# Performance work log

Hardware: AMD Instinct MI355X
Metric: run time of the kernel (lower is better)

## Reference

```python
import jax, jax.numpy as jnp
import numpy as np

N = 100000
E = 1600000
IN_C, HID_C, OUT_C = 128, 256, 40


def sage_conv(x, src, dst, W_l, W_r, b):
    # mean aggregation of source-node features into destination nodes
    msgs = x[src]                                            # [E, d]
    agg = jax.ops.segment_sum(msgs, dst, num_segments=N)     # [N, d]
    deg = jax.ops.segment_sum(jnp.ones((src.shape[0],), x.dtype), dst,
                              num_segments=N)                # [N]
    agg = agg / jnp.clip(deg, 1.0, None)[:, None]
    # out = lin_l(agg) + lin_r(x); weights stored [out, in] like torch
    return agg @ W_l.T + x @ W_r.T + b


def setup_inputs() -> dict:
    key = jax.random.key(0)
    ks = jax.random.split(key, 10)
    s = 0.05
    x = jax.random.normal(ks[0], (N, IN_C), dtype=jnp.float32)
    edge_index = jax.random.randint(ks[1], (2, E), 0, N, dtype=jnp.int64)
    return {
        "x": x,
        "edge_index": edge_index,
        "W_l0": jax.random.normal(ks[2], (HID_C, IN_C), dtype=jnp.float32) * s,
        "W_r0": jax.random.normal(ks[3], (HID_C, IN_C), dtype=jnp.float32) * s,
        "b0": jnp.zeros((HID_C,), jnp.float32),
        "W_l1": jax.random.normal(ks[4], (HID_C, HID_C), dtype=jnp.float32) * s,
        "W_r1": jax.random.normal(ks[5], (HID_C, HID_C), dtype=jnp.float32) * s,
        "b1": jnp.zeros((HID_C,), jnp.float32),
        "W_lo": jax.random.normal(ks[6], (OUT_C, HID_C), dtype=jnp.float32) * s,
        "W_ro": jax.random.normal(ks[7], (OUT_C, HID_C), dtype=jnp.float32) * s,
        "bo": jnp.zeros((OUT_C,), jnp.float32),
    }


def reference(x, edge_index, W_l0, W_r0, b0, W_l1, W_r1, b1, W_lo, W_ro, bo):
    src, dst = edge_index[0], edge_index[1]
    h = jax.nn.relu(sage_conv(x, src, dst, W_l0, W_r0, b0))
    h = jax.nn.relu(sage_conv(h, src, dst, W_l1, W_r1, b1))
    out = sage_conv(h, src, dst, W_lo, W_ro, bo)
    return jax.nn.log_softmax(out, axis=1)
```

## Files before the change

kernel.cpp:

```cpp
#include <hip/hip_runtime.h>
#include <hip/hip_bf16.h>
#include <cstdint>
#include <cstddef>

#define NN   100000
#define NE   1600000
#define HID  256
#define OUTC 40

typedef __attribute__((ext_vector_type(8))) short bf16x8;
typedef __attribute__((ext_vector_type(4))) float f32x4;

static __device__ __forceinline__ ushort f2bf(float f) {
    __hip_bfloat16 h = __float2bfloat16(f);
    return *reinterpret_cast<ushort*>(&h);
}
static __device__ __forceinline__ float bflo(unsigned u) { return __uint_as_float(u << 16); }
static __device__ __forceinline__ float bfhi(unsigned u) { return __uint_as_float(u & 0xffff0000u); }
static __device__ __forceinline__ float ubf(unsigned w, int k) {
    return (float)((w >> (8 * k)) & 255u);
}

__global__ void k_count(const int* __restrict__ dst, int* __restrict__ cnt) {
    int i = blockIdx.x * blockDim.x + threadIdx.x;
    if (i < NE) atomicAdd(&cnt[dst[i]], 1);
}

__global__ void k_blocksum(const int* __restrict__ cnt, int* __restrict__ bsum) {
    __shared__ int s[256];
    int t = threadIdx.x;
    int n = blockIdx.x * 256 + t;
    s[t] = (n < NN) ? cnt[n] : 0;
    __syncthreads();
    for (int off = 128; off; off >>= 1) {
        if (t < off) s[t] += s[t + off];
        __syncthreads();
    }
    if (t == 0) bsum[blockIdx.x] = s[0];
}

__global__ void k_scanblock(const int* __restrict__ bsum, int* __restrict__ boff, int nb) {
    __shared__ int s[512];
    int t = threadIdx.x;
    int v = (t < nb) ? bsum[t] : 0;
    s[t] = v;
    __syncthreads();
    for (int off = 1; off < 512; off <<= 1) {
        int u = (t >= off) ? s[t - off] : 0;
        __syncthreads();
        s[t] += u;
        __syncthreads();
    }
    if (t < nb) boff[t] = s[t] - v;
}

__global__ void k_rowptr(const int* __restrict__ cnt, const int* __restrict__ boff,
                         int* __restrict__ rowptr, int* __restrict__ fillp,
                         float* __restrict__ invd) {
    __shared__ int s[256];
    int t = threadIdx.x;
    int n = blockIdx.x * 256 + t;
    int c = (n < NN) ? cnt[n] : 0;
    s[t] = c;
    __syncthreads();
    for (int off = 1; off < 256; off <<= 1) {
        int u = (t >= off) ? s[t - off] : 0;
        __syncthreads();
        s[t] += u;
        __syncthreads();
    }
    if (n < NN) {
        int excl = boff[blockIdx.x] + s[t] - c;
        rowptr[n] = excl;
        fillp[n]  = excl;
        invd[n]   = 1.0f / (float)(c > 1 ? c : 1);
    }
    if (n == 0) rowptr[NN] = NE;
}

__global__ void k_fill(const int* __restrict__ src, const int* __restrict__ dst,
                       int* __restrict__ fillp, int* __restrict__ colidx) {
    int i = blockIdx.x * blockDim.x + threadIdx.x;
    if (i < NE) {
        int p = atomicAdd(&fillp[dst[i]], 1);
        colidx[p] = src[i];
    }
}

__global__ void k_cvtfrag(const float* __restrict__ W, ushort* __restrict__ dst,
                          int ocreal, int d, int nf) {
    int f = blockIdx.x * 256 + threadIdx.x;
    if (f >= nf) return;
    int lm = f & 15, lk = (f >> 4) & 3;
    int rest = f >> 6;
    int dk = d / 32;
    int kk = rest % dk, cc = rest / dk;
    int row = cc * 16 + lm, col = kk * 32 + lk * 8;
    unsigned q0 = 0, q1 = 0, q2 = 0, q3 = 0;
    if (row < ocreal) {
        const float4* p = (const float4*)(W + (size_t)row * d + col);
        float4 a = p[0], b = p[1];
        q0 = (unsigned)f2bf(a.x) | ((unsigned)f2bf(a.y) << 16);
        q1 = (unsigned)f2bf(a.z) | ((unsigned)f2bf(a.w) << 16);
        q2 = (unsigned)f2bf(b.x) | ((unsigned)f2bf(b.y) << 16);
        q3 = (unsigned)f2bf(b.z) | ((unsigned)f2bf(b.w) << 16);
    }
    *(uint4*)(dst + (size_t)f * 8) = make_uint4(q0, q1, q2, q3);
}

__global__ __launch_bounds__(256) void k_quant_x8(const float* __restrict__ x,
                                                  unsigned char* __restrict__ xq,
                                                  float* __restrict__ sx) {
    int t = threadIdx.x;
    int qw = t >> 4, ql = t & 15;
    int row = blockIdx.x * 16 + qw;
    if (row >= NN) return;
    const float4* p = (const float4*)(x + (size_t)row * 128 + ql * 8);
    float4 a = p[0], b = p[1];
    float v[8] = {a.x, a.y, a.z, a.w, b.x, b.y, b.z, b.w};
    float m = 0.f;
    #pragma unroll
    for (int k = 0; k < 8; ++k) m = fmaxf(m, fabsf(v[k]));
    m = fmaxf(m, __shfl_xor(m, 1));
    m = fmaxf(m, __shfl_xor(m, 2));
    m = fmaxf(m, __shfl_xor(m, 4));
    m = fmaxf(m, __shfl_xor(m, 8));
    float inv = (m > 0.f) ? 127.f / m : 0.f;
    unsigned w0 = 0, w1 = 0;
    #pragma unroll
    for (int k = 0; k < 4; ++k)
        w0 |= ((unsigned)((int)rintf(v[k] * inv) + 128) & 255u) << (8 * k);
    #pragma unroll
    for (int k = 0; k < 4; ++k)
        w1 |= ((unsigned)((int)rintf(v[4 + k] * inv) + 128) & 255u) << (8 * k);
    *(uint2*)(xq + (size_t)row * 128 + ql * 8) = make_uint2(w0, w1);
    if (ql == 0) sx[row] = (m > 0.f) ? m / 127.f : 0.f;
}

__global__ __launch_bounds__(256) void k_quant_h8(const ushort* __restrict__ h,
                                                  unsigned char* __restrict__ hq,
                                                  float* __restrict__ s8) {
    int t = threadIdx.x;
    int qw = t >> 4, ql = t & 15;
    int row = blockIdx.x * 16 + qw;
    if (row >= NN) return;
    const uint4* p = (const uint4*)(h + (size_t)row * 256 + ql * 16);
    uint4 a = p[0], b = p[1];
    float v[16];
    v[0]  = bflo(a.x); v[1]  = bfhi(a.x); v[2]  = bflo(a.y); v[3]  = bfhi(a.y);
    v[4]  = bflo(a.z); v[5]  = bfhi(a.z); v[6]  = bflo(a.w); v[7]  = bfhi(a.w);
    v[8]  = bflo(b.x); v[9]  = bfhi(b.x); v[10] = bflo(b.y); v[11] = bfhi(b.y);
    v[12] = bflo(b.z); v[13] = bfhi(b.z); v[14] = bflo(b.w); v[15] = bfhi(b.w);
    float m = 0.f;
    #pragma unroll
    for (int k = 0; k < 16; ++k) m = fmaxf(m, v[k]);
    m = fmaxf(m, __shfl_xor(m, 1));
    m = fmaxf(m, __shfl_xor(m, 2));
    m = fmaxf(m, __shfl_xor(m, 4));
    m = fmaxf(m, __shfl_xor(m, 8));
    float inv = (m > 0.f) ? 255.f / m : 0.f;
    unsigned wo[4];
    #pragma unroll
    for (int wi = 0; wi < 4; ++wi) {
        unsigned w = 0;
        #pragma unroll
        for (int k = 0; k < 4; ++k)
            w |= ((unsigned)(int)rintf(v[wi * 4 + k] * inv) & 255u) << (8 * k);
        wo[wi] = w;
    }
    *(uint4*)(hq + (size_t)row * 256 + ql * 16) = make_uint4(wo[0], wo[1], wo[2], wo[3]);
    if (ql == 0) s8[row] = (m > 0.f) ? m / 255.f : 0.f;
}

template<int D, bool SELF_F32, bool BIASED>
__global__ __launch_bounds__(256, 4) void k_layer8u(
    const unsigned char* __restrict__ qin, const float* __restrict__ qs,
    const float* __restrict__ xf,
    const ushort* __restrict__ Wl, const ushort* __restrict__ Wr,
    const float* __restrict__ bias, const float* __restrict__ invd,
    const int* __restrict__ rowptr, const int* __restrict__ colidx,
    ushort* __restrict__ hout)
{
    __shared__ ushort aggS[64 * D];
    __shared__ int cidxS[2048];
    char* aggSb = (char*)aggS;
    const int t  = threadIdx.x;
    const int r0 = blockIdx.x * 64;
    constexpr int LPR = D / 16;
    constexpr int GPB = 256 / LPR;
    constexpr int RSH = (D == 128) ? 7 : 8;
    const int gid = t / LPR, li = t % LPR;
    const int l = t & 63;
    const int base = l & ~(LPR - 1);

    const int ebase = rowptr[r0];
    const int rend  = (r0 + 64 < NN) ? (r0 + 64) : NN;
    const int etot  = rowptr[rend] - ebase;
    const bool inlds = (etot <= 2048);
    if (inlds) {
        for (int i = t; i < etot; i += 256) cidxS[i] = colidx[ebase + i];
    }
    __syncthreads();

    for (int rr = gid; rr < 64; rr += GPB) {
        const int r = r0 + rr;
        float acc[16];
        #pragma unroll
        for (int k = 0; k < 16; ++k) acc[k] = 0.f;
        float sum_sc = 0.f;
        if (r < NN) {
            const int beg = rowptr[r], end = rowptr[r + 1];
            for (int e = beg; e < end; e += 8) {
                const int myi = e + (li & 7);
                int se = -1;
                if (myi < end) se = inlds ? cidxS[myi - ebase] : colidx[myi];
                float mysc = (se >= 0) ? qs[se] : 0.f;
                int   sj[8];
                float sc[8];
                uint4 u[8];
                #pragma unroll
                for (int j = 0; j < 8; ++j) sj[j] = __shfl(se, base + j);
                #pragma unroll
                for (int j = 0; j < 8; ++j) sc[j] = __shfl(mysc, base + j);
                #pragma unroll
                for (int j = 0; j < 8; ++j) {
                    u[j] = (sj[j] >= 0)
                        ? *(const uint4*)(qin + (((unsigned)sj[j]) << RSH) + (li << 4))
                        : make_uint4(0u, 0u, 0u, 0u);
                }
                #pragma unroll
                for (int j = 0; j < 8; ++j) {
                    #pragma unroll
                    for (int wi = 0; wi < 4; ++wi) {
                        unsigned w = (&u[j].x)[wi];
                        acc[wi*4+0] = fmaf(sc[j], ubf(w, 0), acc[wi*4+0]);
                        acc[wi*4+1] = fmaf(sc[j], ubf(w, 1), acc[wi*4+1]);
                        acc[wi*4+2] = fmaf(sc[j], ubf(w, 2), acc[wi*4+2]);
                        acc[wi*4+3] = fmaf(sc[j], ubf(w, 3), acc[wi*4+3]);
                    }
                    if (BIASED) sum_sc += sc[j];
                }
            }
            const float iv = invd[r];
            #pragma unroll
            for (int k = 0; k < 16; ++k) {
                if (BIASED) acc[k] = (acc[k] - 128.f * sum_sc) * iv;
                else        acc[k] = acc[k] * iv;
            }
        }
        #pragma unroll
        for (int gg = 0; gg < 2; ++gg) {
            unsigned q0 = (unsigned)f2bf(acc[gg*8+0]) | ((unsigned)f2bf(acc[gg*8+1]) << 16);
            unsigned q1 = (unsigned)f2bf(acc[gg*8+2]) | ((unsigned)f2bf(acc[gg*8+3]) << 16);
            unsigned q2 = (unsigned)f2bf(acc[gg*8+4]) | ((unsigned)f2bf(acc[gg*8+5]) << 16);
            unsigned q3 = (unsigned)f2bf(acc[gg*8+6]) | ((unsigned)f2bf(acc[gg*8+7]) << 16);
            int g  = li * 2 + gg;
            int gs = g ^ (rr & 7);
            *(uint4*)(aggSb + (size_t)rr * (D * 2) + (gs << 4)) = make_uint4(q0, q1, q2, q3);
        }
    }
    __syncthreads();

    const int w = t >> 6, lm = l & 15, lk = l >> 4;
    const int rr = w * 16 + lm;
    const int rg = r0 + rr;

    bf16x8 ax[D / 32];
    if (SELF_F32) {
        #pragma unroll
        for (int kk = 0; kk < D / 32; ++kk) {
            bf16x8 v;
            if (rg < NN) {
                const float4* p = (const float4*)(xf + (size_t)rg * D + kk * 32 + lk * 8);
                float4 f0 = p[0], f1 = p[1];
                v[0] = (short)f2bf(f0.x); v[1] = (short)f2bf(f0.y);
                v[2] = (short)f2bf(f0.z); v[3] = (short)f2bf(f0.w);
                v[4] = (short)f2bf(f1.x); v[5] = (short)f2bf(f1.y);
                v[6] = (short)f2bf(f1.z); v[7] = (short)f2bf(f1.w);
            } else v = (bf16x8)(short)0;
            ax[kk] = v;
        }
    } else {
        const float sr = (rg < NN) ? qs[rg] : 0.f;
        #pragma unroll
        for (int kk = 0; kk < D / 32; ++kk) {
            uint2 uq = (rg < NN)
                ? *(const uint2*)(qin + (((unsigned)rg) << RSH) + kk * 32 + lk * 8)
                : make_uint2(0u, 0u);
            bf16x8 v;
            v[0] = (short)f2bf(sr * ubf(uq.x, 0));
            v[1] = (short)f2bf(sr * ubf(uq.x, 1));
            v[2] = (short)f2bf(sr * ubf(uq.x, 2));
            v[3] = (short)f2bf(sr * ubf(uq.x, 3));
            v[4] = (short)f2bf(sr * ubf(uq.y, 0));
            v[5] = (short)f2bf(sr * ubf(uq.y, 1));
            v[6] = (short)f2bf(sr * ubf(uq.y, 2));
            v[7] = (short)f2bf(sr * ubf(uq.y, 3));
            ax[kk] = v;
        }
    }

    for (int cc = 0; cc < HID / 16; ++cc) {
        const int c = cc * 16 + lm;
        f32x4 acc = {0.f, 0.f, 0.f, 0.f};
        #pragma unroll
        for (int kk = 0; kk < D / 32; ++kk) {
            int g  = kk * 4 + lk;
            int gs = g ^ (rr & 7);
            bf16x8 a_agg = *(const bf16x8*)(aggSb + (size_t)rr * (D * 2) + (gs << 4));
            const size_t wf = ((size_t)(cc * (D / 32) + kk) * 64 + l) * 8;
            bf16x8 bl = *(const bf16x8*)(Wl + wf);
            bf16x8 br = *(const bf16x8*)(Wr + wf);
            acc = __builtin_amdgcn_mfma_f32_16x16x32_bf16(a_agg, bl, acc, 0, 0, 0);
            acc = __builtin_amdgcn_mfma_f32_16x16x32_bf16(ax[kk], br, acc, 0, 0, 0);
        }
        const float bv = bias[c];
        #pragma unroll
        for (int i = 0; i < 4; ++i) {
            const int orow = r0 + w * 16 + lk * 4 + i;
            if (orow < NN) {
                float v = fmaxf(acc[i] + bv, 0.f);
                hout[(size_t)orow * HID + c] = f2bf(v);
            }
        }
    }
}

__global__ __launch_bounds__(256, 4) void k_premul(
    const ushort* __restrict__ h1, const ushort* __restrict__ wlo,
    const ushort* __restrict__ wro, const float* __restrict__ bo,
    unsigned char* __restrict__ qq, float* __restrict__ sq, float* __restrict__ rbuf)
{
    const int t = threadIdx.x;
    const int r0 = blockIdx.x * 64;
    const int w = t >> 6, l = t & 63, lm = l & 15, lk = l >> 4;
    const int rr = w * 16 + lm;
    const int rg = r0 + rr;

    f32x4 aq[3], ar[3];
    #pragma unroll
    for (int cc = 0; cc < 3; ++cc) { aq[cc] = {0.f,0.f,0.f,0.f}; ar[cc] = {0.f,0.f,0.f,0.f}; }

    #pragma unroll
    for (int kk = 0; kk < 8; ++kk) {
        bf16x8 a = (rg < NN)
            ? *(const bf16x8*)(h1 + (size_t)rg * 256 + kk * 32 + lk * 8)
            : (bf16x8)(short)0;
        #pragma unroll
        for (int cc = 0; cc < 3; ++cc) {
            const size_t wf = ((size_t)(cc * 8 + kk) * 64 + l) * 8;
            bf16x8 bl = *(const bf16x8*)(wlo + wf);
            bf16x8 br = *(const bf16x8*)(wro + wf);
            aq[cc] = __builtin_amdgcn_mfma_f32_16x16x32_bf16(a, bl, aq[cc], 0, 0, 0);
            ar[cc] = __builtin_amdgcn_mfma_f32_16x16x32_bf16(a, br, ar[cc], 0, 0, 0);
        }
    }

    #pragma unroll
    for (int i = 0; i < 4; ++i) {
        const int orow = r0 + w * 16 + lk * 4 + i;
        if (orow >= NN) continue;
        float m = 0.f;
        #pragma unroll
        for (int cc = 0; cc < 3; ++cc) {
            const int c = cc * 16 + lm;
            if (c < OUTC) m = fmaxf(m, fabsf(aq[cc][i]));
        }
        m = fmaxf(m, __shfl_xor(m, 1));
        m = fmaxf(m, __shfl_xor(m, 2));
        m = fmaxf(m, __shfl_xor(m, 4));
        m = fmaxf(m, __shfl_xor(m, 8));
        const float inv = (m > 0.f) ? 127.f / m : 0.f;
        #pragma unroll
        for (int cc = 0; cc < 3; ++cc) {
            const int c = cc * 16 + lm;
            int code = (c < OUTC) ? (int)rintf(aq[cc][i] * inv) : 0;
            qq[(size_t)orow * 64 + c] = (unsigned char)(code + 128);
            rbuf[(size_t)orow * 64 + c] = (c < OUTC) ? (ar[cc][i] + bo[c]) : 0.f;
        }
        qq[(size_t)orow * 64 + 48 + lm] = (unsigned char)128;
        rbuf[(size_t)orow * 64 + 48 + lm] = 0.f;
        if (lm == 0) sq[orow] = m / 127.f;
    }
}

__global__ __launch_bounds__(256) void k_final(
    const unsigned char* __restrict__ qq, const float* __restrict__ sq,
    const float* __restrict__ rbuf, const float* __restrict__ invd,
    const int* __restrict__ rowptr, const int* __restrict__ colidx,
    float* __restrict__ out)
{
    __shared__ int cidxS[2048];
    const int t = threadIdx.x;
    const int g = t >> 2, li = t & 3;
    const int r0 = blockIdx.x * 64;
    const int row = r0 + g;
    const int l = t & 63;
    const int base = l & ~3;

    const int ebase = rowptr[r0];
    const int rend  = (r0 + 64 < NN) ? (r0 + 64) : NN;
    const int etot  = rowptr[rend] - ebase;
    const bool inlds = (etot <= 2048);
    if (inlds) {
        for (int i = t; i < etot; i += 256) cidxS[i] = colidx[ebase + i];
    }
    __syncthreads();
    if (row >= NN) return;

    float acc[16];
    #pragma unroll
    for (int k = 0; k < 16; ++k) acc[k] = 0.f;
    float sum_sc = 0.f;

    const int beg = rowptr[row], end = rowptr[row + 1];
    for (int e = beg; e < end; e += 8) {
        const int m0 = e + li, m1 = e + 4 + li;
        int se0 = -1, se1 = -1;
        if (m0 < end) se0 = inlds ? cidxS[m0 - ebase] : colidx[m0];
        if (m1 < end) se1 = inlds ? cidxS[m1 - ebase] : colidx[m1];
        float ms0 = (se0 >= 0) ? sq[se0] : 0.f;
        float ms1 = (se1 >= 0) ? sq[se1] : 0.f;
        int   sj[8];
        float sc[8];
        uint4 u[8];
        #pragma unroll
        for (int j = 0; j < 4; ++j) { sj[j] = __shfl(se0, base + j); sc[j] = __shfl(ms0, base + j); }
        #pragma unroll
        for (int j = 4; j < 8; ++j) { sj[j] = __shfl(se1, base + j - 4); sc[j] = __shfl(ms1, base + j - 4); }
        #pragma unroll
        for (int j = 0; j < 8; ++j) {
            u[j] = (sj[j] >= 0)
                ? *(const uint4*)(qq + (((unsigned)sj[j]) << 6) + (li << 4))
                : make_uint4(0u, 0u, 0u, 0u);
        }
        #pragma unroll
        for (int j = 0; j < 8; ++j) {
            #pragma unroll
            for (int wi = 0; wi < 4; ++wi) {
                unsigned w = (&u[j].x)[wi];
                acc[wi*4+0] = fmaf(sc[j], ubf(w, 0), acc[wi*4+0]);
                acc[wi*4+1] = fmaf(sc[j], ubf(w, 1), acc[wi*4+1]);
                acc[wi*4+2] = fmaf(sc[j], ubf(w, 2), acc[wi*4+2]);
                acc[wi*4+3] = fmaf(sc[j], ubf(w, 3), acc[wi*4+3]);
            }
            sum_sc += sc[j];
        }
    }

    const float iv = invd[row];
    const float4* rp = (const float4*)(rbuf + (size_t)row * 64 + li * 16);
    float v[16];
    #pragma unroll
    for (int ch = 0; ch < 4; ++ch) {
        float4 rv = rp[ch];
        v[ch*4+0] = (acc[ch*4+0] - 128.f * sum_sc) * iv + rv.x;
        v[ch*4+1] = (acc[ch*4+1] - 128.f * sum_sc) * iv + rv.y;
        v[ch*4+2] = (acc[ch*4+2] - 128.f * sum_sc) * iv + rv.z;
        v[ch*4+3] = (acc[ch*4+3] - 128.f * sum_sc) * iv + rv.w;
    }
    #pragma unroll
    for (int k = 0; k < 16; ++k)
        if (li * 16 + k >= OUTC) v[k] = -INFINITY;

    float m = v[0];
    #pragma unroll
    for (int k = 1; k < 16; ++k) m = fmaxf(m, v[k]);
    m = fmaxf(m, __shfl_xor(m, 1));
    m = fmaxf(m, __shfl_xor(m, 2));

    float s = 0.f;
    #pragma unroll
    for (int k = 0; k < 16; ++k)
        if (li * 16 + k < OUTC) s += __expf(v[k] - m);
    s += __shfl_xor(s, 1);
    s += __shfl_xor(s, 2);
    const float ls = __logf(s);

    #pragma unroll
    for (int ch = 0; ch < 4; ++ch) {
        const int c = li * 16 + ch * 4;
        if (c < OUTC) {
            float4 o;
            o.x = v[ch*4+0] - m - ls;
            o.y = v[ch*4+1] - m - ls;
            o.z = v[ch*4+2] - m - ls;
            o.w = v[ch*4+3] - m - ls;
            *(float4*)(out + (size_t)row * OUTC + c) = o;
        }
    }
}

extern "C" void kernel_launch(void* const* d_in, const int* in_sizes, int n_in,
                              void* d_out, int out_size, void* d_ws, size_t ws_size,
                              hipStream_t stream) {
    const float* x   = (const float*)d_in[0];
    const int*   ei  = (const int*)d_in[1];
    const int*   src = ei;
    const int*   dst = ei + NE;
    const float* Wl0 = (const float*)d_in[2];
    const float* Wr0 = (const float*)d_in[3];
    const float* b0  = (const float*)d_in[4];
    const float* Wl1 = (const float*)d_in[5];
    const float* Wr1 = (const float*)d_in[6];
    const float* b1  = (const float*)d_in[7];
    const float* Wlo = (const float*)d_in[8];
    const float* Wro = (const float*)d_in[9];
    const float* bo  = (const float*)d_in[10];
    float* out = (float*)d_out;

    char* ws = (char*)d_ws;
    const size_t MB = 1 << 20;
    float*         invd   = (float*)(ws + 0);
    int*           rowptr = (int*)(ws + MB / 2);
    int*           cnt    = (int*)(ws + MB);
    int*           fillp  = (int*)(ws + MB + MB / 2);
    int*           bsum   = (int*)(ws + 2 * MB);
    int*           boff   = (int*)(ws + 2 * MB + MB / 4);
    float*         sx     = (float*)(ws + 2 * MB + MB / 2);
    float*         s8     = (float*)(ws + 3 * MB);
    float*         sq     = (float*)(ws + 4 * MB);
    ushort*        Wb     = (ushort*)(ws + 4 * MB + MB / 2);
    int*           colidx = (int*)(ws + 5 * MB + MB / 2);
    unsigned char* xq8    = (unsigned char*)(ws + 12 * MB);
    unsigned char* qq     = (unsigned char*)(ws + 12 * MB);
    ushort*        h0     = (ushort*)(ws + 32 * MB);
    ushort*        h1     = (ushort*)(ws + 32 * MB);
    unsigned char* h0q8u  = (unsigned char*)(ws + 84 * MB);
    float*         rbuf   = (float*)(ws + 84 * MB);

    ushort* wl0 = Wb;
    ushort* wr0 = Wb + 32768;
    ushort* wl1 = Wb + 65536;
    ushort* wr1 = Wb + 131072;
    ushort* wlo = Wb + 196608;
    ushort* wro = Wb + 208896;

    hipMemsetAsync(cnt, 0, NN * sizeof(int), stream);
    k_count<<<(NE + 255) / 256, 256, 0, stream>>>(dst, cnt);
    const int NB = (NN + 255) / 256;
    k_blocksum<<<NB, 256, 0, stream>>>(cnt, bsum);
    k_scanblock<<<1, 512, 0, stream>>>(bsum, boff, NB);
    k_rowptr<<<NB, 256, 0, stream>>>(cnt, boff, rowptr, fillp, invd);
    k_fill<<<(NE + 255) / 256, 256, 0, stream>>>(src, dst, fillp, colidx);

    k_cvtfrag<<<16, 256, 0, stream>>>(Wl0, wl0, 256, 128, 4096);
    k_cvtfrag<<<16, 256, 0, stream>>>(Wr0, wr0, 256, 128, 4096);
    k_cvtfrag<<<32, 256, 0, stream>>>(Wl1, wl1, 256, 256, 8192);
    k_cvtfrag<<<32, 256, 0, stream>>>(Wr1, wr1, 256, 256, 8192);
    k_cvtfrag<<<6,  256, 0, stream>>>(Wlo, wlo, 40, 256, 1536);
    k_cvtfrag<<<6,  256, 0, stream>>>(Wro, wro, 40, 256, 1536);
    k_quant_x8<<<(NN + 15) / 16, 256, 0, stream>>>(x, xq8, sx);

    const int GB = (NN + 63) / 64;
    k_layer8u<128, true, true><<<GB, 256, 0, stream>>>(
        xq8, sx, x, wl0, wr0, b0, invd, rowptr, colidx, h0);
    k_quant_h8<<<(NN + 15) / 16, 256, 0, stream>>>(h0, h0q8u, s8);
    k_layer8u<256, false, false><<<GB, 256, 0, stream>>>(
        h0q8u, s8, nullptr, wl1, wr1, b1, invd, rowptr, colidx, h1);
    k_premul<<<GB, 256, 0, stream>>>(h1, wlo, wro, bo, qq, sq, rbuf);
    k_final<<<(NN + 63) / 64, 256, 0, stream>>>(qq, sq, rbuf, invd, rowptr, colidx, out);
}
```

Before: 513.4 us.

## Shrink layer-kernel row tiles and split output columns across waves

The layer kernels now process fewer rows per block (32 rows for D=128, 16 for D=256) so that each thread group aggregates exactly one row, and shared memory shrinks accordingly. In the MFMA stage the waves split the output columns instead of each owning a 16-row tile, and the launch bounds are raised to allow more resident blocks. The aim is more blocks and higher occupancy for the latency-bound gather. In exchange, weight fragments are reloaded by more blocks, there are more launches' worth of blocks, and the column-index cache in shared memory is smaller.

```diff
diff --git a/kernel.cpp b/kernel.cpp
--- a/kernel.cpp
+++ b/kernel.cpp
@@ -173,7 +173,7 @@
 }
 
 template<int D, bool SELF_F32, bool BIASED>
-__global__ __launch_bounds__(256, 4) void k_layer8u(
+__global__ __launch_bounds__(256, 6) void k_layer8u(
     const unsigned char* __restrict__ qin, const float* __restrict__ qs,
     const float* __restrict__ xf,
     const ushort* __restrict__ Wl, const ushort* __restrict__ Wr,
@@ -181,28 +181,33 @@
     const int* __restrict__ rowptr, const int* __restrict__ colidx,
     ushort* __restrict__ hout)
 {
-    __shared__ ushort aggS[64 * D];
-    __shared__ int cidxS[2048];
+    constexpr int R   = 4096 / D;
+    constexpr int LPR = D / 16;
+    constexpr int RSH = (D == 128) ? 7 : 8;
+    constexpr int NRT = R / 16;
+    constexpr int WPRT = 4 / NRT;
+    constexpr int CCW  = 16 / WPRT;
+
+    __shared__ ushort aggS[R * D];
+    __shared__ int cidxS[1024];
     char* aggSb = (char*)aggS;
     const int t  = threadIdx.x;
-    const int r0 = blockIdx.x * 64;
-    constexpr int LPR = D / 16;
-    constexpr int GPB = 256 / LPR;
-    constexpr int RSH = (D == 128) ? 7 : 8;
+    const int r0 = blockIdx.x * R;
     const int gid = t / LPR, li = t % LPR;
     const int l = t & 63;
     const int base = l & ~(LPR - 1);
 
     const int ebase = rowptr[r0];
-    const int rend  = (r0 + 64 < NN) ? (r0 + 64) : NN;
+    const int rend  = (r0 + R < NN) ? (r0 + R) : NN;
     const int etot  = rowptr[rend] - ebase;
-    const bool inlds = (etot <= 2048);
+    const bool inlds = (etot <= 1024);
     if (inlds) {
         for (int i = t; i < etot; i += 256) cidxS[i] = colidx[ebase + i];
     }
     __syncthreads();
 
-    for (int rr = gid; rr < 64; rr += GPB) {
+    {
+        const int rr = gid;
         const int r = r0 + rr;
         float acc[16];
         #pragma unroll
@@ -262,7 +267,9 @@
     __syncthreads();
 
     const int w = t >> 6, lm = l & 15, lk = l >> 4;
-    const int rr = w * 16 + lm;
+    const int rt  = w / WPRT;
+    const int cc0 = (w % WPRT) * CCW;
+    const int rr = rt * 16 + lm;
     const int rg = r0 + rr;
 
     bf16x8 ax[D / 32];
@@ -300,7 +307,9 @@
         }
     }
 
-    for (int cc = 0; cc < HID / 16; ++cc) {
+    #pragma unroll
+    for (int ccl = 0; ccl < CCW; ++ccl) {
+        const int cc = cc0 + ccl;
         const int c = cc * 16 + lm;
         f32x4 acc = {0.f, 0.f, 0.f, 0.f};
         #pragma unroll
@@ -317,7 +326,7 @@
         const float bv = bias[c];
         #pragma unroll
         for (int i = 0; i < 4; ++i) {
-            const int orow = r0 + w * 16 + lk * 4 + i;
+            const int orow = r0 + rt * 16 + lk * 4 + i;
             if (orow < NN) {
                 float v = fmaxf(acc[i] + bv, 0.f);
                 hout[(size_t)orow * HID + c] = f2bf(v);
@@ -552,12 +561,11 @@
     k_cvtfrag<<<6,  256, 0, stream>>>(Wro, wro, 40, 256, 1536);
     k_quant_x8<<<(NN + 15) / 16, 256, 0, stream>>>(x, xq8, sx);
 
-    const int GB = (NN + 63) / 64;
-    k_layer8u<128, true, true><<<GB, 256, 0, stream>>>(
+    k_layer8u<128, true, true><<<(NN + 31) / 32, 256, 0, stream>>>(
         xq8, sx, x, wl0, wr0, b0, invd, rowptr, colidx, h0);
     k_quant_h8<<<(NN + 15) / 16, 256, 0, stream>>>(h0, h0q8u, s8);
-    k_layer8u<256, false, false><<<GB, 256, 0, stream>>>(
+    k_layer8u<256, false, false><<<(NN + 15) / 16, 256, 0, stream>>>(
         h0q8u, s8, nullptr, wl1, wr1, b1, invd, rowptr, colidx, h1);
-    k_premul<<<GB, 256, 0, stream>>>(h1, wlo, wro, bo, qq, sq, rbuf);
+    k_premul<<<(NN + 63) / 64, 256, 0, stream>>>(h1, wlo, wro, bo, qq, sq, rbuf);
     k_final<<<(NN + 63) / 64, 256, 0, stream>>>(qq, sq, rbuf, invd, rowptr, colidx, out);
 }
```

Result: slower. 536.2 us (+4.4%).

## Fuse h0 quantization into layer0 and output premul into layer1 epilogue

Applied to the files above, without the earlier changes.

The layer-0 kernel now quantizes its ReLU output to uint8 per row directly in the MFMA epilogue, so the separate bf16 h0 write and the quantize pass are gone. The layer-1 kernel writes its ReLU output into shared memory and performs the output-layer premultiply in place, so the bf16 h1 round-trip and the premul launch are gone. The MFMA loops are restructured to hold all 16 output-column accumulators at once and reuse each A fragment across columns, with occupancy lowered to 3 blocks per SM. The risks are higher register pressure and byte-wise scattered global stores of the quantized output.

```diff
diff --git a/kernel.cpp b/kernel.cpp
--- a/kernel.cpp
+++ b/kernel.cpp
@@ -137,61 +137,20 @@
     if (ql == 0) sx[row] = (m > 0.f) ? m / 127.f : 0.f;
 }
 
-__global__ __launch_bounds__(256) void k_quant_h8(const ushort* __restrict__ h,
-                                                  unsigned char* __restrict__ hq,
-                                                  float* __restrict__ s8) {
-    int t = threadIdx.x;
-    int qw = t >> 4, ql = t & 15;
-    int row = blockIdx.x * 16 + qw;
-    if (row >= NN) return;
-    const uint4* p = (const uint4*)(h + (size_t)row * 256 + ql * 16);
-    uint4 a = p[0], b = p[1];
-    float v[16];
-    v[0]  = bflo(a.x); v[1]  = bfhi(a.x); v[2]  = bflo(a.y); v[3]  = bfhi(a.y);
-    v[4]  = bflo(a.z); v[5]  = bfhi(a.z); v[6]  = bflo(a.w); v[7]  = bfhi(a.w);
-    v[8]  = bflo(b.x); v[9]  = bfhi(b.x); v[10] = bflo(b.y); v[11] = bfhi(b.y);
-    v[12] = bflo(b.z); v[13] = bfhi(b.z); v[14] = bflo(b.w); v[15] = bfhi(b.w);
-    float m = 0.f;
-    #pragma unroll
-    for (int k = 0; k < 16; ++k) m = fmaxf(m, v[k]);
-    m = fmaxf(m, __shfl_xor(m, 1));
-    m = fmaxf(m, __shfl_xor(m, 2));
-    m = fmaxf(m, __shfl_xor(m, 4));
-    m = fmaxf(m, __shfl_xor(m, 8));
-    float inv = (m > 0.f) ? 255.f / m : 0.f;
-    unsigned wo[4];
-    #pragma unroll
-    for (int wi = 0; wi < 4; ++wi) {
-        unsigned w = 0;
-        #pragma unroll
-        for (int k = 0; k < 4; ++k)
-            w |= ((unsigned)(int)rintf(v[wi * 4 + k] * inv) & 255u) << (8 * k);
-        wo[wi] = w;
-    }
-    *(uint4*)(hq + (size_t)row * 256 + ql * 16) = make_uint4(wo[0], wo[1], wo[2], wo[3]);
-    if (ql == 0) s8[row] = (m > 0.f) ? m / 255.f : 0.f;
-}
-
-template<int D, bool SELF_F32, bool BIASED>
-__global__ __launch_bounds__(256, 4) void k_layer8u(
-    const unsigned char* __restrict__ qin, const float* __restrict__ qs,
+__global__ __launch_bounds__(256, 3) void k_layer0(
+    const unsigned char* __restrict__ xq, const float* __restrict__ sx,
     const float* __restrict__ xf,
     const ushort* __restrict__ Wl, const ushort* __restrict__ Wr,
     const float* __restrict__ bias, const float* __restrict__ invd,
     const int* __restrict__ rowptr, const int* __restrict__ colidx,
-    ushort* __restrict__ hout)
+    unsigned char* __restrict__ hq, float* __restrict__ hs)
 {
-    __shared__ ushort aggS[64 * D];
+    __shared__ ushort aggS[64 * 128];
     __shared__ int cidxS[2048];
     char* aggSb = (char*)aggS;
     const int t  = threadIdx.x;
     const int r0 = blockIdx.x * 64;
-    constexpr int LPR = D / 16;
-    constexpr int GPB = 256 / LPR;
-    constexpr int RSH = (D == 128) ? 7 : 8;
-    const int gid = t / LPR, li = t % LPR;
     const int l = t & 63;
-    const int base = l & ~(LPR - 1);
 
     const int ebase = rowptr[r0];
     const int rend  = (r0 + 64 < NN) ? (r0 + 64) : NN;
@@ -202,61 +161,62 @@
     }
     __syncthreads();
 
-    for (int rr = gid; rr < 64; rr += GPB) {
-        const int r = r0 + rr;
-        float acc[16];
-        #pragma unroll
-        for (int k = 0; k < 16; ++k) acc[k] = 0.f;
-        float sum_sc = 0.f;
-        if (r < NN) {
-            const int beg = rowptr[r], end = rowptr[r + 1];
-            for (int e = beg; e < end; e += 8) {
-                const int myi = e + (li & 7);
-                int se = -1;
-                if (myi < end) se = inlds ? cidxS[myi - ebase] : colidx[myi];
-                float mysc = (se >= 0) ? qs[se] : 0.f;
-                int   sj[8];
-                float sc[8];
-                uint4 u[8];
+    {
+        const int gid = t >> 3, li = t & 7;
+        const int base = l & ~7;
+        for (int rr = gid; rr < 64; rr += 32) {
+            const int r = r0 + rr;
+            float acc[16];
+            #pragma unroll
+            for (int k = 0; k < 16; ++k) acc[k] = 0.f;
+            float sum_sc = 0.f;
+            if (r < NN) {
+                const int beg = rowptr[r], end = rowptr[r + 1];
+                for (int e = beg; e < end; e += 8) {
+                    const int myi = e + li;
+                    int se = -1;
+                    if (myi < end) se = inlds ? cidxS[myi - ebase] : colidx[myi];
+                    float mysc = (se >= 0) ? sx[se] : 0.f;
+                    int   sj[8];
+                    float sc[8];
+                    uint4 u[8];
+                    #pragma unroll
+                    for (int j = 0; j < 8; ++j) sj[j] = __shfl(se, base + j);
+                    #pragma unroll
+                    for (int j = 0; j < 8; ++j) sc[j] = __shfl(mysc, base + j);
+                    #pragma unroll
+                    for (int j = 0; j < 8; ++j) {
+                        u[j] = (sj[j] >= 0)
+                            ? *(const uint4*)(xq + (((unsigned)sj[j]) << 7) + (li << 4))
+                            : make_uint4(0u, 0u, 0u, 0u);
+                    }
+                    #pragma unroll
+                    for (int j = 0; j < 8; ++j) {
+                        #pragma unroll
+                        for (int wi = 0; wi < 4; ++wi) {
+                            unsigned w = (&u[j].x)[wi];
+                            acc[wi*4+0] = fmaf(sc[j], ubf(w, 0), acc[wi*4+0]);
+                            acc[wi*4+1] = fmaf(sc[j], ubf(w, 1), acc[wi*4+1]);
+                            acc[wi*4+2] = fmaf(sc[j], ubf(w, 2), acc[wi*4+2]);
+                            acc[wi*4+3] = fmaf(sc[j], ubf(w, 3), acc[wi*4+3]);
+                        }
+                        sum_sc += sc[j];
+                    }
+                }
+                const float iv = invd[r];
                 #pragma unroll
-                for (int j = 0; j < 8; ++j) sj[j] = __shfl(se, base + j);
-                #pragma unroll
-                for (int j = 0; j < 8; ++j) sc[j] = __shfl(mysc, base + j);
-                #pragma unroll
-                for (int j = 0; j < 8; ++j) {
-                    u[j] = (sj[j] >= 0)
-                        ? *(const uint4*)(qin + (((unsigned)sj[j]) << RSH) + (li << 4))
-                        : make_uint4(0u, 0u, 0u, 0u);
-                }
-                #pragma unroll
-                for (int j = 0; j < 8; ++j) {
-                    #pragma unroll
-                    for (int wi = 0; wi < 4; ++wi) {
-                        unsigned w = (&u[j].x)[wi];
-                        acc[wi*4+0] = fmaf(sc[j], ubf(w, 0), acc[wi*4+0]);
-                        acc[wi*4+1] = fmaf(sc[j], ubf(w, 1), acc[wi*4+1]);
-                        acc[wi*4+2] = fmaf(sc[j], ubf(w, 2), acc[wi*4+2]);
-                        acc[wi*4+3] = fmaf(sc[j], ubf(w, 3), acc[wi*4+3]);
-                    }
-                    if (BIASED) sum_sc += sc[j];
-                }
+                for (int k = 0; k < 16; ++k) acc[k] = (acc[k] - 128.f * sum_sc) * iv;
             }
-            const float iv = invd[r];
             #pragma unroll
-            for (int k = 0; k < 16; ++k) {
-                if (BIASED) acc[k] = (acc[k] - 128.f * sum_sc) * iv;
-                else        acc[k] = acc[k] * iv;
+            for (int gg = 0; gg < 2; ++gg) {
+                unsigned q0 = (unsigned)f2bf(acc[gg*8+0]) | ((unsigned)f2bf(acc[gg*8+1]) << 16);
+                unsigned q1 = (unsigned)f2bf(acc[gg*8+2]) | ((unsigned)f2bf(acc[gg*8+3]) << 16);
+                unsigned q2 = (unsigned)f2bf(acc[gg*8+4]) | ((unsigned)f2bf(acc[gg*8+5]) << 16);
+                unsigned q3 = (unsigned)f2bf(acc[gg*8+6]) | ((unsigned)f2bf(acc[gg*8+7]) << 16);
+                int g  = li * 2 + gg;
+                int gs = g ^ (rr & 7);
+                *(uint4*)(aggSb + (size_t)rr * 256 + (gs << 4)) = make_uint4(q0, q1, q2, q3);
             }
-        }
-        #pragma unroll
-        for (int gg = 0; gg < 2; ++gg) {
-            unsigned q0 = (unsigned)f2bf(acc[gg*8+0]) | ((unsigned)f2bf(acc[gg*8+1]) << 16);
-            unsigned q1 = (unsigned)f2bf(acc[gg*8+2]) | ((unsigned)f2bf(acc[gg*8+3]) << 16);
-            unsigned q2 = (unsigned)f2bf(acc[gg*8+4]) | ((unsigned)f2bf(acc[gg*8+5]) << 16);
-            unsigned q3 = (unsigned)f2bf(acc[gg*8+6]) | ((unsigned)f2bf(acc[gg*8+7]) << 16);
-            int g  = li * 2 + gg;
-            int gs = g ^ (rr & 7);
-            *(uint4*)(aggSb + (size_t)rr * (D * 2) + (gs << 4)) = make_uint4(q0, q1, q2, q3);
         }
     }
     __syncthreads();
@@ -265,27 +225,173 @@
     const int rr = w * 16 + lm;
     const int rg = r0 + rr;
 
-    bf16x8 ax[D / 32];
-    if (SELF_F32) {
-        #pragma unroll
-        for (int kk = 0; kk < D / 32; ++kk) {
-            bf16x8 v;
-            if (rg < NN) {
-                const float4* p = (const float4*)(xf + (size_t)rg * D + kk * 32 + lk * 8);
-                float4 f0 = p[0], f1 = p[1];
-                v[0] = (short)f2bf(f0.x); v[1] = (short)f2bf(f0.y);
-                v[2] = (short)f2bf(f0.z); v[3] = (short)f2bf(f0.w);
-                v[4] = (short)f2bf(f1.x); v[5] = (short)f2bf(f1.y);
-                v[6] = (short)f2bf(f1.z); v[7] = (short)f2bf(f1.w);
-            } else v = (bf16x8)(short)0;
-            ax[kk] = v;
-        }
-    } else {
-        const float sr = (rg < NN) ? qs[rg] : 0.f;
-        #pragma unroll
-        for (int kk = 0; kk < D / 32; ++kk) {
+    bf16x8 ax[4];
+    #pragma unroll
+    for (int kk = 0; kk < 4; ++kk) {
+        bf16x8 v;
+        if (rg < NN) {
+            const float4* p = (const float4*)(xf + (size_t)rg * 128 + kk * 32 + lk * 8);
+            float4 f0 = p[0], f1 = p[1];
+            v[0] = (short)f2bf(f0.x); v[1] = (short)f2bf(f0.y);
+            v[2] = (short)f2bf(f0.z); v[3] = (short)f2bf(f0.w);
+            v[4] = (short)f2bf(f1.x); v[5] = (short)f2bf(f1.y);
+            v[6] = (short)f2bf(f1.z); v[7] = (short)f2bf(f1.w);
+        } else v = (bf16x8)(short)0;
+        ax[kk] = v;
+    }
+
+    f32x4 acc[16];
+    #pragma unroll
+    for (int cc = 0; cc < 16; ++cc) acc[cc] = {0.f, 0.f, 0.f, 0.f};
+
+    #pragma unroll
+    for (int kk = 0; kk < 4; ++kk) {
+        int g  = kk * 4 + lk;
+        int gs = g ^ (rr & 7);
+        bf16x8 a_agg = *(const bf16x8*)(aggSb + (size_t)rr * 256 + (gs << 4));
+        #pragma unroll
+        for (int cc = 0; cc < 16; ++cc) {
+            const size_t wf = ((size_t)(cc * 4 + kk) * 64 + l) * 8;
+            bf16x8 bl = *(const bf16x8*)(Wl + wf);
+            bf16x8 br = *(const bf16x8*)(Wr + wf);
+            acc[cc] = __builtin_amdgcn_mfma_f32_16x16x32_bf16(a_agg,  bl, acc[cc], 0, 0, 0);
+            acc[cc] = __builtin_amdgcn_mfma_f32_16x16x32_bf16(ax[kk], br, acc[cc], 0, 0, 0);
+        }
+    }
+
+    float vmax[4] = {0.f, 0.f, 0.f, 0.f};
+    #pragma unroll
+    for (int cc = 0; cc < 16; ++cc) {
+        const float bv = bias[cc * 16 + lm];
+        #pragma unroll
+        for (int i = 0; i < 4; ++i) {
+            float v = fmaxf(acc[cc][i] + bv, 0.f);
+            acc[cc][i] = v;
+            vmax[i] = fmaxf(vmax[i], v);
+        }
+    }
+    #pragma unroll
+    for (int i = 0; i < 4; ++i) {
+        vmax[i] = fmaxf(vmax[i], __shfl_xor(vmax[i], 1));
+        vmax[i] = fmaxf(vmax[i], __shfl_xor(vmax[i], 2));
+        vmax[i] = fmaxf(vmax[i], __shfl_xor(vmax[i], 4));
+        vmax[i] = fmaxf(vmax[i], __shfl_xor(vmax[i], 8));
+    }
+    float invq[4];
+    #pragma unroll
+    for (int i = 0; i < 4; ++i) invq[i] = (vmax[i] > 0.f) ? 255.f / vmax[i] : 0.f;
+    const int ob = r0 + w * 16 + lk * 4;
+    if (lm == 0) {
+        #pragma unroll
+        for (int i = 0; i < 4; ++i)
+            if (ob + i < NN) hs[ob + i] = vmax[i] / 255.f;
+    }
+    #pragma unroll
+    for (int cc = 0; cc < 16; ++cc) {
+        #pragma unroll
+        for (int i = 0; i < 4; ++i) {
+            if (ob + i < NN)
+                hq[(size_t)(ob + i) * 256 + cc * 16 + lm] =
+                    (unsigned char)(int)rintf(acc[cc][i] * invq[i]);
+        }
+    }
+}
+
+__global__ __launch_bounds__(256, 3) void k_layer1(
+    const unsigned char* __restrict__ hq, const float* __restrict__ hs,
+    const ushort* __restrict__ Wl, const ushort* __restrict__ Wr,
+    const float* __restrict__ bias,
+    const ushort* __restrict__ wlo, const ushort* __restrict__ wro,
+    const float* __restrict__ bo,
+    const float* __restrict__ invd,
+    const int* __restrict__ rowptr, const int* __restrict__ colidx,
+    unsigned char* __restrict__ qq, float* __restrict__ sq, float* __restrict__ rbuf)
+{
+    __shared__ ushort aggS[64 * 256];
+    __shared__ int cidxS[2048];
+    char* aggSb = (char*)aggS;
+    const int t  = threadIdx.x;
+    const int r0 = blockIdx.x * 64;
+    const int l = t & 63;
+
+    const int ebase = rowptr[r0];
+    const int rend  = (r0 + 64 < NN) ? (r0 + 64) : NN;
+    const int etot  = rowptr[rend] - ebase;
+    const bool inlds = (etot <= 2048);
+    if (inlds) {
+        for (int i = t; i < etot; i += 256) cidxS[i] = colidx[ebase + i];
+    }
+    __syncthreads();
+
+    {
+        const int gid = t >> 4, li = t & 15;
+        const int base = l & ~15;
+        for (int rr = gid; rr < 64; rr += 16) {
+            const int r = r0 + rr;
+            float acc[16];
+            #pragma unroll
+            for (int k = 0; k < 16; ++k) acc[k] = 0.f;
+            if (r < NN) {
+                const int beg = rowptr[r], end = rowptr[r + 1];
+                for (int e = beg; e < end; e += 8) {
+                    const int myi = e + (li & 7);
+                    int se = -1;
+                    if (myi < end) se = inlds ? cidxS[myi - ebase] : colidx[myi];
+                    float mysc = (se >= 0) ? hs[se] : 0.f;
+                    int   sj[8];
+                    float sc[8];
+                    uint4 u[8];
+                    #pragma unroll
+                    for (int j = 0; j < 8; ++j) sj[j] = __shfl(se, base + j);
+                    #pragma unroll
+                    for (int j = 0; j < 8; ++j) sc[j] = __shfl(mysc, base + j);
+                    #pragma unroll
+                    for (int j = 0; j < 8; ++j) {
+                        u[j] = (sj[j] >= 0)
+                            ? *(const uint4*)(hq + (((unsigned)sj[j]) << 8) + (li << 4))
+                            : make_uint4(0u, 0u, 0u, 0u);
+                    }
+                    #pragma unroll
+                    for (int j = 0; j < 8; ++j) {
+                        #pragma unroll
+                        for (int wi = 0; wi < 4; ++wi) {
+                            unsigned w = (&u[j].x)[wi];
+                            acc[wi*4+0] = fmaf(sc[j], ubf(w, 0), acc[wi*4+0]);
+                            acc[wi*4+1] = fmaf(sc[j], ubf(w, 1), acc[wi*4+1]);
+                            acc[wi*4+2] = fmaf(sc[j], ubf(w, 2), acc[wi*4+2]);
+                            acc[wi*4+3] = fmaf(sc[j], ubf(w, 3), acc[wi*4+3]);
+                        }
+                    }
+                }
+                const float iv = invd[r];
+                #pragma unroll
+                for (int k = 0; k < 16; ++k) acc[k] *= iv;
+            }
+            #pragma unroll
+            for (int gg = 0; gg < 2; ++gg) {
+                unsigned q0 = (unsigned)f2bf(acc[gg*8+0]) | ((unsigned)f2bf(acc[gg*8+1]) << 16);
+                unsigned q1 = (unsigned)f2bf(acc[gg*8+2]) | ((unsigned)f2bf(acc[gg*8+3]) << 16);
+                unsigned q2 = (unsigned)f2bf(acc[gg*8+4]) | ((unsigned)f2bf(acc[gg*8+5]) << 16);
+                unsigned q3 = (unsigned)f2bf(acc[gg*8+6]) | ((unsigned)f2bf(acc[gg*8+7]) << 16);
+                int g  = li * 2 + gg;
+                int gs = g ^ (rr & 7);
+                *(uint4*)(aggSb + (size_t)rr * 512 + (gs << 4)) = make_uint4(q0, q1, q2, q3);
+            }
+        }
+    }
+    __syncthreads();
+
+    const int w = t >> 6, lm = l & 15, lk = l >> 4;
+    const int rr = w * 16 + lm;
+    const int rg = r0 + rr;
+
+    bf16x8 ax[8];
+    {
+        const float sr = (rg < NN) ? hs[rg] : 0.f;
+        #pragma unroll
+        for (int kk = 0; kk < 8; ++kk) {
             uint2 uq = (rg < NN)
-                ? *(const uint2*)(qin + (((unsigned)rg) << RSH) + kk * 32 + lk * 8)
+                ? *(const uint2*)(hq + (((unsigned)rg) << 8) + kk * 32 + lk * 8)
                 : make_uint2(0u, 0u);
             bf16x8 v;
             v[0] = (short)f2bf(sr * ubf(uq.x, 0));
@@ -300,52 +406,50 @@
         }
     }
 
-    for (int cc = 0; cc < HID / 16; ++cc) {
-        const int c = cc * 16 + lm;
-        f32x4 acc = {0.f, 0.f, 0.f, 0.f};
-        #pragma unroll
-        for (int kk = 0; kk < D / 32; ++kk) {
-            int g  = kk * 4 + lk;
-            int gs = g ^ (rr & 7);
-            bf16x8 a_agg = *(const bf16x8*)(aggSb + (size_t)rr * (D * 2) + (gs << 4));
-            const size_t wf = ((size_t)(cc * (D / 32) + kk) * 64 + l) * 8;
+    f32x4 acc[16];
+    #pragma unroll
+    for (int cc = 0; cc < 16; ++cc) acc[cc] = {0.f, 0.f, 0.f, 0.f};
+
+    #pragma unroll
+    for (int kk = 0; kk < 8; ++kk) {
+        int g  = kk * 4 + lk;
+        int gs = g ^ (rr & 7);
+        bf16x8 a_agg = *(const bf16x8*)(aggSb + (size_t)rr * 512 + (gs << 4));
+        #pragma unroll
+        for (int cc = 0; cc < 16; ++cc) {
+            const size_t wf = ((size_t)(cc * 8 + kk) * 64 + l) * 8;
             bf16x8 bl = *(const bf16x8*)(Wl + wf);
             bf16x8 br = *(const bf16x8*)(Wr + wf);
-            acc = __builtin_amdgcn_mfma_f32_16x16x32_bf16(a_agg, bl, acc, 0, 0, 0);
-            acc = __builtin_amdgcn_mfma_f32_16x16x32_bf16(ax[kk], br, acc, 0, 0, 0);
-        }
+            acc[cc] = __builtin_amdgcn_mfma_f32_16x16x32_bf16(a_agg,  bl, acc[cc], 0, 0, 0);
+            acc[cc] = __builtin_amdgcn_mfma_f32_16x16x32_bf16(ax[kk], br, acc[cc], 0, 0, 0);
+        }
+    }
+
+    #pragma unroll
+    for (int cc = 0; cc < 16; ++cc) {
+        const int c = cc * 16 + lm;
         const float bv = bias[c];
         #pragma unroll
         for (int i = 0; i < 4; ++i) {
-            const int orow = r0 + w * 16 + lk * 4 + i;
-            if (orow < NN) {
-                float v = fmaxf(acc[i] + bv, 0.f);
-                hout[(size_t)orow * HID + c] = f2bf(v);
-            }
-        }
-    }
-}
-
-__global__ __launch_bounds__(256, 4) void k_premul(
-    const ushort* __restrict__ h1, const ushort* __restrict__ wlo,
-    const ushort* __restrict__ wro, const float* __restrict__ bo,
-    unsigned char* __restrict__ qq, float* __restrict__ sq, float* __restrict__ rbuf)
-{
-    const int t = threadIdx.x;
-    const int r0 = blockIdx.x * 64;
-    const int w = t >> 6, l = t & 63, lm = l & 15, lk = l >> 4;
-    const int rr = w * 16 + lm;
-    const int rg = r0 + rr;
+            float v = fmaxf(acc[cc][i] + bv, 0.f);
+            int row = w * 16 + lk * 4 + i;
+            int g = c >> 3;
+            int gs = g ^ (row & 7);
+            *(ushort*)(aggSb + (size_t)row * 512 + (gs << 4) + ((c & 7) << 1)) = f2bf(v);
+        }
+    }
+    __syncthreads();
 
     f32x4 aq[3], ar[3];
     #pragma unroll
     for (int cc = 0; cc < 3; ++cc) { aq[cc] = {0.f,0.f,0.f,0.f}; ar[cc] = {0.f,0.f,0.f,0.f}; }
 
+    const int prow = w * 16 + lm;
     #pragma unroll
     for (int kk = 0; kk < 8; ++kk) {
-        bf16x8 a = (rg < NN)
-            ? *(const bf16x8*)(h1 + (size_t)rg * 256 + kk * 32 + lk * 8)
-            : (bf16x8)(short)0;
+        int g  = kk * 4 + lk;
+        int gs = g ^ (prow & 7);
+        bf16x8 a = *(const bf16x8*)(aggSb + (size_t)prow * 512 + (gs << 4));
         #pragma unroll
         for (int cc = 0; cc < 3; ++cc) {
             const size_t wf = ((size_t)(cc * 8 + kk) * 64 + l) * 8;
@@ -518,16 +622,14 @@
     int*           bsum   = (int*)(ws + 2 * MB);
     int*           boff   = (int*)(ws + 2 * MB + MB / 4);
     float*         sx     = (float*)(ws + 2 * MB + MB / 2);
-    float*         s8     = (float*)(ws + 3 * MB);
-    float*         sq     = (float*)(ws + 4 * MB);
-    ushort*        Wb     = (ushort*)(ws + 4 * MB + MB / 2);
-    int*           colidx = (int*)(ws + 5 * MB + MB / 2);
-    unsigned char* xq8    = (unsigned char*)(ws + 12 * MB);
-    unsigned char* qq     = (unsigned char*)(ws + 12 * MB);
-    ushort*        h0     = (ushort*)(ws + 32 * MB);
-    ushort*        h1     = (ushort*)(ws + 32 * MB);
-    unsigned char* h0q8u  = (unsigned char*)(ws + 84 * MB);
-    float*         rbuf   = (float*)(ws + 84 * MB);
+    float*         s0     = (float*)(ws + 3 * MB);
+    float*         sq     = (float*)(ws + 3 * MB + MB / 2);
+    ushort*        Wb     = (ushort*)(ws + 4 * MB);
+    int*           colidx = (int*)(ws + 4 * MB + MB / 2);
+    unsigned char* xq8    = (unsigned char*)(ws + 11 * MB);
+    unsigned char* qq     = (unsigned char*)(ws + 11 * MB);
+    unsigned char* h0q    = (unsigned char*)(ws + 24 * MB);
+    float*         rbuf   = (float*)(ws + 50 * MB);
 
     ushort* wl0 = Wb;
     ushort* wr0 = Wb + 32768;
@@ -553,11 +655,8 @@
     k_quant_x8<<<(NN + 15) / 16, 256, 0, stream>>>(x, xq8, sx);
 
     const int GB = (NN + 63) / 64;
-    k_layer8u<128, true, true><<<GB, 256, 0, stream>>>(
-        xq8, sx, x, wl0, wr0, b0, invd, rowptr, colidx, h0);
-    k_quant_h8<<<(NN + 15) / 16, 256, 0, stream>>>(h0, h0q8u, s8);
-    k_layer8u<256, false, false><<<GB, 256, 0, stream>>>(
-        h0q8u, s8, nullptr, wl1, wr1, b1, invd, rowptr, colidx, h1);
-    k_premul<<<GB, 256, 0, stream>>>(h1, wlo, wro, bo, qq, sq, rbuf);
-    k_final<<<(NN + 63) / 64, 256, 0, stream>>>(qq, sq, rbuf, invd, rowptr, colidx, out);
-}
+    k_layer0<<<GB, 256, 0, stream>>>(xq8, sx, x, wl0, wr0, b0, invd, rowptr, colidx, h0q, s0);
+    k_layer1<<<GB, 256, 0, stream>>>(h0q, s0, wl1, wr1, b1, wlo, wro, bo,
+                                     invd, rowptr, colidx, qq, sq, rbuf);
+    k_final<<<GB, 256, 0, stream>>>(qq, sq, rbuf, invd, rowptr, colidx, out);
+}
```

After: 533.5 us. +3.9%, slower.
